# Optimization experiments

Measured on AMD Instinct MI355X. Metric: run time of the kernel, lower is better.

Reference implementation:

```python
import jax, jax.numpy as jnp
import numpy as np
from jax import lax

SEQ = 32768
I = 128   # input_size
H = 512   # hidden_layer_size


def lstm_scan(xs, W_ih, W_hh, b_ih, b_hh):
    """Single-layer LSTM over time (PyTorch gate order i,f,g,o), batch=1.
    xs: [T, in], W_ih: [4h, in], W_hh: [4h, h], biases: [4h]. Returns [T, h]."""
    h_dim = W_hh.shape[1]
    x_gates = xs @ W_ih.T + (b_ih + b_hh)  # precompute input contribution [T, 4h]

    def step(carry, xg):
        h, c = carry
        gates = xg + h @ W_hh.T
        i, f, g, o = jnp.split(gates, 4)
        i = jax.nn.sigmoid(i)
        f = jax.nn.sigmoid(f)
        g = jnp.tanh(g)
        o = jax.nn.sigmoid(o)
        c = f * c + i * g
        h = o * jnp.tanh(c)
        return (h, c), h

    init = (jnp.zeros((h_dim,), xs.dtype), jnp.zeros((h_dim,), xs.dtype))
    _, hs = lax.scan(step, init, x_gates)
    return hs


def setup_inputs() -> dict:
    key = jax.random.key(0)
    ks = jax.random.split(key, 9)
    u = lambda k, shape, fan: jax.random.uniform(k, shape, jnp.float32, -1.0, 1.0) / np.sqrt(fan)
    return {
        "input_seq": jax.random.normal(ks[0], (SEQ, I), jnp.float32),
        # layer 1: input I -> hidden H
        "W_ih1": u(ks[1], (4 * H, I), H),
        "W_hh1": u(ks[2], (4 * H, H), H),
        "b_ih1": u(ks[3], (4 * H,), H),
        "b_hh1": u(ks[4], (4 * H,), H),
        # layer 2: hidden H -> input I
        "W_ih2": u(ks[5], (4 * I, H), I),
        "W_hh2": u(ks[6], (4 * I, I), I),
        "b_ih2": u(ks[7], (4 * I,), I),
        "b_hh2": u(ks[8], (4 * I,), I),
    }


def reference(input_seq, W_ih1, W_hh1, b_ih1, b_hh1, W_ih2, W_hh2, b_ih2, b_hh2):
    h1 = lstm_scan(input_seq, W_ih1, W_hh1, b_ih1, b_hh1)   # [T, H]
    h2 = lstm_scan(h1, W_ih2, W_hh2, b_ih2, b_hh2)          # [T, I]
    return h2.reshape(-1)                                    # predictions.view(-1)
```

## Files before the change

### kernel.cpp

```cpp
#include <hip/hip_runtime.h>
#include <math.h>


#define T_STEPS 32768
#define L1WG    16
#define NWG     24
#define BLK     512
#define GRID    192
#define RD      8

#define ABT_OFF  9
#define TAG_OFF  32
#define H1F_OFF  1024
#define H1S_OFF  (H1F_OFF + RD * 512 * 2)
#define H2F_OFF  (H1S_OFF + RD * 512 * 2)
#define H2S_OFF  (H2F_OFF + RD * 128 * 2)
#define WS_WORDS (H2S_OFF + RD * 128 * 2)

typedef unsigned int uint4v __attribute__((ext_vector_type(4)));

__device__ __forceinline__ float sigm(float x) { return 1.0f / (1.0f + __expf(-x)); }
__device__ __forceinline__ float tanh_fast(float x) { return 1.0f - 2.0f / (__expf(2.0f * x) + 1.0f); }

__device__ __forceinline__ unsigned ld_u32_sc1(const unsigned* p) {
    unsigned r;
    asm volatile("global_load_dword %0, %1, off sc1\n\ts_waitcnt vmcnt(0)"
                 : "=v"(r) : "v"(p) : "memory");
    return r;
}
__device__ __forceinline__ void st_u32_sc1(unsigned* p, unsigned v) {
    asm volatile("global_store_dword %0, %1, off sc1" :: "v"(p), "v"(v) : "memory");
}
__device__ __forceinline__ void st_u64_sc0(unsigned long long* p, unsigned long long v) {
    asm volatile("global_store_dwordx2 %0, %1, off sc0" :: "v"(p), "v"(v) : "memory");
}
__device__ __forceinline__ void st_u64_sc1(unsigned long long* p, unsigned long long v) {
    asm volatile("global_store_dwordx2 %0, %1, off sc1" :: "v"(p), "v"(v) : "memory");
}
__device__ __forceinline__ void ld2x16_sc0(const unsigned long long* p, uint4v& A, uint4v& B) {
    asm volatile("global_load_dwordx4 %0, %2, off sc0\n\t"
                 "global_load_dwordx4 %1, %3, off sc0\n\t"
                 "s_waitcnt vmcnt(0)"
                 : "=&v"(A), "=&v"(B) : "v"(p), "v"(p + 2) : "memory");
}
__device__ __forceinline__ void ld2x16_sc1(const unsigned long long* p, uint4v& A, uint4v& B) {
    asm volatile("global_load_dwordx4 %0, %2, off sc1\n\t"
                 "global_load_dwordx4 %1, %3, off sc1\n\t"
                 "s_waitcnt vmcnt(0)"
                 : "=&v"(A), "=&v"(B) : "v"(p), "v"(p + 2) : "memory");
}
__device__ __forceinline__ void ld1x16_sc0(const unsigned long long* p, uint4v& A) {
    asm volatile("global_load_dwordx4 %0, %1, off sc0\n\ts_waitcnt vmcnt(0)"
                 : "=&v"(A) : "v"(p) : "memory");
}
__device__ __forceinline__ void ld1x16_sc1(const unsigned long long* p, uint4v& A) {
    asm volatile("global_load_dwordx4 %0, %1, off sc1\n\ts_waitcnt vmcnt(0)"
                 : "=&v"(A) : "v"(p) : "memory");
}

__global__ void lstm_init(unsigned int* ws)
{
    int i = blockIdx.x * blockDim.x + threadIdx.x;
    if (i < WS_WORDS) ws[i] = 0u;
}

__global__ __launch_bounds__(BLK) void lstm_persist(
    const float* __restrict__ x,
    const float* __restrict__ Wih1,
    const float* __restrict__ Whh1,
    const float* __restrict__ bih1,
    const float* __restrict__ bhh1,
    const float* __restrict__ Wih2,
    const float* __restrict__ Whh2,
    const float* __restrict__ bih2,
    const float* __restrict__ bhh2,
    float* __restrict__ out,
    unsigned int* ws)
{
    const int bid = blockIdx.x;
    if (bid & 7) return;
    const int role = bid >> 3;
    if (role >= NWG) return;

    const int tid  = threadIdx.x;
    const int wave = tid >> 6;
    const int lane = tid & 63;

    __shared__ __align__(16) float h1buf[2][16 * 36];
    __shared__ __align__(16) float h2buf[2][8 * 20];
    __shared__ unsigned s_ab[1];

    unsigned* abf  = ws + ABT_OFF;
    unsigned* tags = ws + TAG_OFF;
    unsigned long long* h1f = (unsigned long long*)(ws + H1F_OFF);
    unsigned long long* h1s = (unsigned long long*)(ws + H1S_OFF);
    unsigned long long* h2f = (unsigned long long*)(ws + H2F_OFF);
    unsigned long long* h2s = (unsigned long long*)(ws + H2S_OFF);

    if (tid == 0) s_ab[0] = 0u;

    const bool isL1 = role < L1WG;

    if (isL1) {
        const int rt = tid >> 4;
        const int ct = tid & 15;
        const int hb = role * 32;

        float wA[4][32], wB[4][8], bia[4];
#pragma unroll
        for (int q = 0; q < 4; ++q) {
            const int grow = q * 512 + hb + rt;
            const float4* pa = (const float4*)(Whh1 + (size_t)grow * 512 + ct * 32);
#pragma unroll
            for (int c = 0; c < 8; ++c) {
                float4 f = pa[c];
                wA[q][c * 4 + 0] = f.x; wA[q][c * 4 + 1] = f.y;
                wA[q][c * 4 + 2] = f.z; wA[q][c * 4 + 3] = f.w;
            }
            const float4* pb = (const float4*)(Wih1 + (size_t)grow * 128 + ct * 8);
            float4 b0 = pb[0], b1 = pb[1];
            wB[q][0] = b0.x; wB[q][1] = b0.y; wB[q][2] = b0.z; wB[q][3] = b0.w;
            wB[q][4] = b1.x; wB[q][5] = b1.y; wB[q][6] = b1.z; wB[q][7] = b1.w;
            bia[q] = bih1[grow] + bhh1[grow];
        }

        float cst = 0.0f;
        float4 vx0 = *(const float4*)(x + ct * 8);
        float4 vx1 = *(const float4*)(x + ct * 8 + 4);
        __syncthreads();

        for (int n = 0; n < T_STEPS; ++n) {
            if (wave == 3 && n >= 7 && lane < NWG) {
                const int thr = n - 6;
                unsigned sp = 0;
                for (;;) {
                    int ok = ((int)ld_u32_sc1(&tags[lane]) >= thr);
                    if (__all(ok)) break;
                    if ((++sp & 255u) == 0u) {
                        if (ld_u32_sc1(abf) != 0u) { s_ab[0] = 1u; break; }
                        if (sp >= (1u << 21)) { st_u32_sc1(abf, 1u); s_ab[0] = 1u; break; }
                    }
                }
            }
            if (wave < 2) {
                const size_t off = (size_t)((n - 1) & (RD - 1)) * 512 + wave * 256 + lane * 4;
                const unsigned long long* pf = h1f + off;
                const unsigned long long* ps = h1s + off;
                const unsigned e = (unsigned)n;
                uint4v A, B;
                unsigned sp = 0;
                for (;;) {
                    ld2x16_sc0(pf, A, B);
                    int ok = (A.y == e) & (A.w == e) & (B.y == e) & (B.w == e);
                    if (__all(ok)) break;
                    if ((++sp & 7u) == 0u) {
                        uint4v C, D;
                        ld2x16_sc1(ps, C, D);
                        if (A.y != e) { A.x = C.x; A.y = C.y; }
                        if (A.w != e) { A.z = C.z; A.w = C.w; }
                        if (B.y != e) { B.x = D.x; B.y = D.y; }
                        if (B.w != e) { B.z = D.z; B.w = D.w; }
                        ok = (A.y == e) & (A.w == e) & (B.y == e) & (B.w == e);
                        if (__all(ok)) break;
                        if ((sp & 2047u) == 0u) {
                            if (ld_u32_sc1(abf) != 0u) { s_ab[0] = 1u; break; }
                            if (sp >= (1u << 22)) { st_u32_sc1(abf, 1u); s_ab[0] = 1u; break; }
                        }
                    }
                }
                const int g = wave * 256 + lane * 4;
                float4 vals = make_float4(__uint_as_float(A.x), __uint_as_float(A.z),
                                          __uint_as_float(B.x), __uint_as_float(B.z));
                *(float4*)&h1buf[n & 1][(g >> 5) * 36 + (g & 31)] = vals;
            }

            __syncthreads();
            if (s_ab[0]) break;
            if (tid == 0) st_u32_sc1(&tags[role], (unsigned)(n + 1));

            float acc0 = 0.f, acc1 = 0.f, acc2 = 0.f, acc3 = 0.f;
            const float* hv = &h1buf[n & 1][ct * 36];
#pragma unroll
            for (int c = 0; c < 8; ++c) {
                float4 h4 = *(const float4*)(hv + c * 4);
                acc0 = fmaf(wA[0][c*4+0], h4.x, acc0); acc0 = fmaf(wA[0][c*4+1], h4.y, acc0);
                acc0 = fmaf(wA[0][c*4+2], h4.z, acc0); acc0 = fmaf(wA[0][c*4+3], h4.w, acc0);
                acc1 = fmaf(wA[1][c*4+0], h4.x, acc1); acc1 = fmaf(wA[1][c*4+1], h4.y, acc1);
                acc1 = fmaf(wA[1][c*4+2], h4.z, acc1); acc1 = fmaf(wA[1][c*4+3], h4.w, acc1);
                acc2 = fmaf(wA[2][c*4+0], h4.x, acc2); acc2 = fmaf(wA[2][c*4+1], h4.y, acc2);
                acc2 = fmaf(wA[2][c*4+2], h4.z, acc2); acc2 = fmaf(wA[2][c*4+3], h4.w, acc2);
                acc3 = fmaf(wA[3][c*4+0], h4.x, acc3); acc3 = fmaf(wA[3][c*4+1], h4.y, acc3);
                acc3 = fmaf(wA[3][c*4+2], h4.z, acc3); acc3 = fmaf(wA[3][c*4+3], h4.w, acc3);
            }
            {
                float sx[8] = { vx0.x, vx0.y, vx0.z, vx0.w, vx1.x, vx1.y, vx1.z, vx1.w };
#pragma unroll
                for (int j = 0; j < 8; ++j) {
                    acc0 = fmaf(wB[0][j], sx[j], acc0);
                    acc1 = fmaf(wB[1][j], sx[j], acc1);
                    acc2 = fmaf(wB[2][j], sx[j], acc2);
                    acc3 = fmaf(wB[3][j], sx[j], acc3);
                }
            }
            {
                const int tn = (n + 1 < T_STEPS) ? (n + 1) : (T_STEPS - 1);
                vx0 = *(const float4*)(x + (size_t)tn * 128 + ct * 8);
                vx1 = *(const float4*)(x + (size_t)tn * 128 + ct * 8 + 4);
            }
#pragma unroll
            for (int m = 8; m >= 1; m >>= 1) {
                acc0 += __shfl_xor(acc0, m, 64);
                acc1 += __shfl_xor(acc1, m, 64);
                acc2 += __shfl_xor(acc2, m, 64);
                acc3 += __shfl_xor(acc3, m, 64);
            }
            const float ii = sigm(acc0 + bia[0]);
            const float ff = sigm(acc1 + bia[1]);
            const float g2 = tanh_fast(acc2 + bia[2]);
            const float oo = sigm(acc3 + bia[3]);
            cst = ff * cst + ii * g2;
            const float h = oo * tanh_fast(cst);

            if (ct == 0) {
                const unsigned long long pair =
                    ((unsigned long long)(unsigned)(n + 1) << 32) |
                    (unsigned long long)__float_as_uint(h);
                const size_t off = (size_t)(n & (RD - 1)) * 512 + hb + rt;
                st_u64_sc0(&h1f[off], pair);
                st_u64_sc1(&h1s[off], pair);
            }
        }
    } else {
        const int rt  = tid >> 5;
        const int ct  = tid & 31;
        const int hb2 = (role - L1WG) * 16;

        float wA[4][16], wB[4][4], bia[4];
#pragma unroll
        for (int q = 0; q < 4; ++q) {
            const int grow = q * 128 + hb2 + rt;
            const float4* pa = (const float4*)(Wih2 + (size_t)grow * 512 + ct * 16);
#pragma unroll
            for (int c = 0; c < 4; ++c) {
                float4 f = pa[c];
                wA[q][c * 4 + 0] = f.x; wA[q][c * 4 + 1] = f.y;
                wA[q][c * 4 + 2] = f.z; wA[q][c * 4 + 3] = f.w;
            }
            float4 b0 = *(const float4*)(Whh2 + (size_t)grow * 128 + ct * 4);
            wB[q][0] = b0.x; wB[q][1] = b0.y; wB[q][2] = b0.z; wB[q][3] = b0.w;
            bia[q] = bih2[grow] + bhh2[grow];
        }

        float cst = 0.0f;
        __syncthreads();

        for (int n = 1; n <= T_STEPS; ++n) {
            const int tau = n - 1;
            if (wave == 3 && n >= 7 && lane < NWG) {
                const int thr = n - 6;
                unsigned sp = 0;
                for (;;) {
                    int ok = ((int)ld_u32_sc1(&tags[lane]) >= thr);
                    if (__all(ok)) break;
                    if ((++sp & 255u) == 0u) {
                        if (ld_u32_sc1(abf) != 0u) { s_ab[0] = 1u; break; }
                        if (sp >= (1u << 21)) { st_u32_sc1(abf, 1u); s_ab[0] = 1u; break; }
                    }
                }
            }
            if (wave < 2) {
                const size_t off = (size_t)(tau & (RD - 1)) * 512 + wave * 256 + lane * 4;
                const unsigned long long* pf = h1f + off;
                const unsigned long long* ps = h1s + off;
                const unsigned e = (unsigned)n;
                uint4v A, B;
                unsigned sp = 0;
                for (;;) {
                    ld2x16_sc0(pf, A, B);
                    int ok = (A.y == e) & (A.w == e) & (B.y == e) & (B.w == e);
                    if (__all(ok)) break;
                    if ((++sp & 7u) == 0u) {
                        uint4v C, D;
                        ld2x16_sc1(ps, C, D);
                        if (A.y != e) { A.x = C.x; A.y = C.y; }
                        if (A.w != e) { A.z = C.z; A.w = C.w; }
                        if (B.y != e) { B.x = D.x; B.y = D.y; }
                        if (B.w != e) { B.z = D.z; B.w = D.w; }
                        ok = (A.y == e) & (A.w == e) & (B.y == e) & (B.w == e);
                        if (__all(ok)) break;
                        if ((sp & 2047u) == 0u) {
                            if (ld_u32_sc1(abf) != 0u) { s_ab[0] = 1u; break; }
                            if (sp >= (1u << 22)) { st_u32_sc1(abf, 1u); s_ab[0] = 1u; break; }
                        }
                    }
                }
                const int g = wave * 256 + lane * 4;
                float4 vals = make_float4(__uint_as_float(A.x), __uint_as_float(A.z),
                                          __uint_as_float(B.x), __uint_as_float(B.z));
                *(float4*)&h1buf[n & 1][(g >> 5) * 36 + (g & 31)] = vals;
            }
            if (wave == 2) {
                const size_t off = (size_t)((tau - 1) & (RD - 1)) * 128 + lane * 2;
                const unsigned long long* pf = h2f + off;
                const unsigned long long* ps = h2s + off;
                const unsigned e = (unsigned)tau;
                uint4v A;
                unsigned sp = 0;
                for (;;) {
                    ld1x16_sc0(pf, A);
                    int ok = (A.y == e) & (A.w == e);
                    if (__all(ok)) break;
                    if ((++sp & 7u) == 0u) {
                        uint4v C;
                        ld1x16_sc1(ps, C);
                        if (A.y != e) { A.x = C.x; A.y = C.y; }
                        if (A.w != e) { A.z = C.z; A.w = C.w; }
                        ok = (A.y == e) & (A.w == e);
                        if (__all(ok)) break;
                        if ((sp & 2047u) == 0u) {
                            if (ld_u32_sc1(abf) != 0u) { s_ab[0] = 1u; break; }
                            if (sp >= (1u << 22)) { st_u32_sc1(abf, 1u); s_ab[0] = 1u; break; }
                        }
                    }
                }
                const int pi = lane * 2;
                float2 v2 = make_float2(__uint_as_float(A.x), __uint_as_float(A.z));
                *(float2*)&h2buf[n & 1][(pi >> 4) * 20 + (pi & 15)] = v2;
            }

            __syncthreads();
            if (s_ab[0]) break;
            if (tid == 0) st_u32_sc1(&tags[role], (unsigned)(n + 1));

            float acc0 = 0.f, acc1 = 0.f, acc2 = 0.f, acc3 = 0.f;
            const float* hv = &h1buf[n & 1][(ct >> 1) * 36 + (ct & 1) * 16];
#pragma unroll
            for (int c = 0; c < 4; ++c) {
                float4 h4 = *(const float4*)(hv + c * 4);
                acc0 = fmaf(wA[0][c*4+0], h4.x, acc0); acc0 = fmaf(wA[0][c*4+1], h4.y, acc0);
                acc0 = fmaf(wA[0][c*4+2], h4.z, acc0); acc0 = fmaf(wA[0][c*4+3], h4.w, acc0);
                acc1 = fmaf(wA[1][c*4+0], h4.x, acc1); acc1 = fmaf(wA[1][c*4+1], h4.y, acc1);
                acc1 = fmaf(wA[1][c*4+2], h4.z, acc1); acc1 = fmaf(wA[1][c*4+3], h4.w, acc1);
                acc2 = fmaf(wA[2][c*4+0], h4.x, acc2); acc2 = fmaf(wA[2][c*4+1], h4.y, acc2);
                acc2 = fmaf(wA[2][c*4+2], h4.z, acc2); acc2 = fmaf(wA[2][c*4+3], h4.w, acc2);
                acc3 = fmaf(wA[3][c*4+0], h4.x, acc3); acc3 = fmaf(wA[3][c*4+1], h4.y, acc3);
                acc3 = fmaf(wA[3][c*4+2], h4.z, acc3); acc3 = fmaf(wA[3][c*4+3], h4.w, acc3);
            }
            {
                float4 s4 = *(const float4*)&h2buf[n & 1][(ct >> 2) * 20 + (ct & 3) * 4];
                float sv[4] = { s4.x, s4.y, s4.z, s4.w };
#pragma unroll
                for (int j = 0; j < 4; ++j) {
                    acc0 = fmaf(wB[0][j], sv[j], acc0);
                    acc1 = fmaf(wB[1][j], sv[j], acc1);
                    acc2 = fmaf(wB[2][j], sv[j], acc2);
                    acc3 = fmaf(wB[3][j], sv[j], acc3);
                }
            }
#pragma unroll
            for (int m = 16; m >= 1; m >>= 1) {
                acc0 += __shfl_xor(acc0, m, 64);
                acc1 += __shfl_xor(acc1, m, 64);
                acc2 += __shfl_xor(acc2, m, 64);
                acc3 += __shfl_xor(acc3, m, 64);
            }
            const float ii = sigm(acc0 + bia[0]);
            const float ff = sigm(acc1 + bia[1]);
            const float g2 = tanh_fast(acc2 + bia[2]);
            const float oo = sigm(acc3 + bia[3]);
            cst = ff * cst + ii * g2;
            const float h = oo * tanh_fast(cst);

            if (ct == 0) {
                const unsigned long long pair =
                    ((unsigned long long)(unsigned)n << 32) |
                    (unsigned long long)__float_as_uint(h);
                const size_t off = (size_t)(tau & (RD - 1)) * 128 + hb2 + rt;
                st_u64_sc0(&h2f[off], pair);
                st_u64_sc1(&h2s[off], pair);
                out[(size_t)tau * 128 + hb2 + rt] = h;
            }
        }
    }
}

extern "C" void kernel_launch(void* const* d_in, const int* in_sizes, int n_in,
                              void* d_out, int out_size, void* d_ws, size_t ws_size,
                              hipStream_t stream)
{
    const float* x    = (const float*)d_in[0];
    const float* Wih1 = (const float*)d_in[1];
    const float* Whh1 = (const float*)d_in[2];
    const float* bih1 = (const float*)d_in[3];
    const float* bhh1 = (const float*)d_in[4];
    const float* Wih2 = (const float*)d_in[5];
    const float* Whh2 = (const float*)d_in[6];
    const float* bih2 = (const float*)d_in[7];
    const float* bhh2 = (const float*)d_in[8];
    unsigned int* ws  = (unsigned int*)d_ws;

    hipLaunchKernelGGL(lstm_init, dim3(96), dim3(256), 0, stream, ws);
    hipLaunchKernelGGL(lstm_persist, dim3(GRID), dim3(BLK), 0, stream,
                       x, Wih1, Whh1, bih1, bhh1, Wih2, Whh2, bih2, bhh2,
                       (float*)d_out, ws);
}
```

Before: 87.85 ms.

## Co-locate all persistent workgroups on one XCD and batch ring-slack checks

Roles are no longer assigned from a fixed block-id stride. Each workgroup reads its XCC id from a hardware register and takes a ticket from a per-XCD atomic counter, and the first XCD to fill all 24 roles wins. This keeps every cross-workgroup flag and h-exchange inside one XCD's L2 rather than crossing dies, which should cut inter-step handoff latency. The grid grows to 256 blocks so one XCD is likely to get 24 of them. The ring-buffer slack wait now runs every 4 steps with threshold n-3 instead of every step with n-6, so it polls less often. In exchange, the assignment adds a startup spin, and if no XCD ever fills the roles, no workgroup takes a role.

```diff
diff --git a/kernel.cpp b/kernel.cpp
--- a/kernel.cpp
+++ b/kernel.cpp
@@ -6,9 +6,11 @@
 #define L1WG    16
 #define NWG     24
 #define BLK     512
-#define GRID    192
+#define GRID    256
 #define RD      8
 
+#define CNT_OFF  0
+#define CHO_OFF  8
 #define ABT_OFF  9
 #define TAG_OFF  32
 #define H1F_OFF  1024
@@ -77,19 +79,17 @@
     float* __restrict__ out,
     unsigned int* ws)
 {
-    const int bid = blockIdx.x;
-    if (bid & 7) return;
-    const int role = bid >> 3;
-    if (role >= NWG) return;
-
     const int tid  = threadIdx.x;
     const int wave = tid >> 6;
     const int lane = tid & 63;
 
     __shared__ __align__(16) float h1buf[2][16 * 36];
     __shared__ __align__(16) float h2buf[2][8 * 20];
+    __shared__ unsigned s_role[1];
     __shared__ unsigned s_ab[1];
 
+    unsigned* cnt  = ws + CNT_OFF;
+    unsigned* cho  = ws + CHO_OFF;
     unsigned* abf  = ws + ABT_OFF;
     unsigned* tags = ws + TAG_OFF;
     unsigned long long* h1f = (unsigned long long*)(ws + H1F_OFF);
@@ -97,7 +97,34 @@
     unsigned long long* h2f = (unsigned long long*)(ws + H2F_OFF);
     unsigned long long* h2s = (unsigned long long*)(ws + H2S_OFF);
 
-    if (tid == 0) s_ab[0] = 0u;
+    if (tid == 0) {
+        s_ab[0] = 0u;
+        unsigned xcc;
+        asm volatile("s_getreg_b32 %0, hwreg(20, 0, 32)" : "=s"(xcc));
+        xcc &= 7u;
+        unsigned role = 0xFFFFu;
+        unsigned tkt = __hip_atomic_fetch_add(&cnt[xcc], 1u,
+                           __ATOMIC_RELAXED, __HIP_MEMORY_SCOPE_AGENT);
+        if (tkt < NWG) {
+            if (tkt == NWG - 1) {
+                unsigned exp = 0u;
+                __hip_atomic_compare_exchange_strong(cho, &exp, xcc + 1u,
+                    __ATOMIC_RELAXED, __ATOMIC_RELAXED, __HIP_MEMORY_SCOPE_AGENT);
+            }
+            unsigned c, sp = 0;
+            for (;;) {
+                c = __hip_atomic_load(cho, __ATOMIC_RELAXED, __HIP_MEMORY_SCOPE_AGENT);
+                if (c != 0u) break;
+                __builtin_amdgcn_s_sleep(2);
+                if (++sp > (1u << 22)) { c = 0xFFu; break; }
+            }
+            if (c == xcc + 1u) role = tkt;
+        }
+        s_role[0] = role;
+    }
+    __syncthreads();
+    const int role = (int)s_role[0];
+    if (role >= NWG) return;
 
     const bool isL1 = role < L1WG;
 
@@ -130,8 +157,8 @@
         __syncthreads();
 
         for (int n = 0; n < T_STEPS; ++n) {
-            if (wave == 3 && n >= 7 && lane < NWG) {
-                const int thr = n - 6;
+            if (wave == 3 && n >= 8 && (n & 3) == 0 && lane < NWG) {
+                const int thr = n - 3;
                 unsigned sp = 0;
                 for (;;) {
                     int ok = ((int)ld_u32_sc1(&tags[lane]) >= thr);
@@ -256,8 +283,8 @@
 
         for (int n = 1; n <= T_STEPS; ++n) {
             const int tau = n - 1;
-            if (wave == 3 && n >= 7 && lane < NWG) {
-                const int thr = n - 6;
+            if (wave == 3 && n >= 8 && (n & 3) == 0 && lane < NWG) {
+                const int thr = n - 3;
                 unsigned sp = 0;
                 for (;;) {
                     int ok = ((int)ld_u32_sc1(&tags[lane]) >= thr);
```

Result: no change. 86.83 ms (-1.2%).

## Use single sc1 ring buffers, per-lane spin with early LDS write, relaxed tag throttling

Applied to the files above, without the earlier changes.

Drops the duplicated fast/slow (sc0/sc1) ring buffers and publishes each hidden value once with an sc1 store. Consumers now poll only the sc1 copy, and each lane writes its value to LDS as soon as its tag matches. The change also checks the run-ahead tags only every fourth step with a tighter lag. It launches exactly 24 blocks instead of 192 with most returning early, and pins weight registers with empty asm. The aim is to cut polling traffic and per-step synchronisation latency. The cost is possible extra cache round-trips from sc1-only loads, and blocks may no longer be spread across distinct XCDs/CUs.

```diff
diff --git a/kernel.cpp b/kernel.cpp
--- a/kernel.cpp
+++ b/kernel.cpp
@@ -6,18 +6,17 @@
 #define L1WG    16
 #define NWG     24
 #define BLK     512
-#define GRID    192
 #define RD      8
 
 #define ABT_OFF  9
 #define TAG_OFF  32
-#define H1F_OFF  1024
-#define H1S_OFF  (H1F_OFF + RD * 512 * 2)
-#define H2F_OFF  (H1S_OFF + RD * 512 * 2)
-#define H2S_OFF  (H2F_OFF + RD * 128 * 2)
-#define WS_WORDS (H2S_OFF + RD * 128 * 2)
+#define H1_OFF   1024
+#define H2_OFF   (H1_OFF + RD * 512 * 2)
+#define WS_WORDS (H2_OFF + RD * 128 * 2)
 
 typedef unsigned int uint4v __attribute__((ext_vector_type(4)));
+
+#define PIN(v) asm volatile("" : "+v"(v))
 
 __device__ __forceinline__ float sigm(float x) { return 1.0f / (1.0f + __expf(-x)); }
 __device__ __forceinline__ float tanh_fast(float x) { return 1.0f - 2.0f / (__expf(2.0f * x) + 1.0f); }
@@ -31,17 +30,8 @@
 __device__ __forceinline__ void st_u32_sc1(unsigned* p, unsigned v) {
     asm volatile("global_store_dword %0, %1, off sc1" :: "v"(p), "v"(v) : "memory");
 }
-__device__ __forceinline__ void st_u64_sc0(unsigned long long* p, unsigned long long v) {
-    asm volatile("global_store_dwordx2 %0, %1, off sc0" :: "v"(p), "v"(v) : "memory");
-}
 __device__ __forceinline__ void st_u64_sc1(unsigned long long* p, unsigned long long v) {
     asm volatile("global_store_dwordx2 %0, %1, off sc1" :: "v"(p), "v"(v) : "memory");
-}
-__device__ __forceinline__ void ld2x16_sc0(const unsigned long long* p, uint4v& A, uint4v& B) {
-    asm volatile("global_load_dwordx4 %0, %2, off sc0\n\t"
-                 "global_load_dwordx4 %1, %3, off sc0\n\t"
-                 "s_waitcnt vmcnt(0)"
-                 : "=&v"(A), "=&v"(B) : "v"(p), "v"(p + 2) : "memory");
 }
 __device__ __forceinline__ void ld2x16_sc1(const unsigned long long* p, uint4v& A, uint4v& B) {
     asm volatile("global_load_dwordx4 %0, %2, off sc1\n\t"
@@ -49,10 +39,6 @@
                  "s_waitcnt vmcnt(0)"
                  : "=&v"(A), "=&v"(B) : "v"(p), "v"(p + 2) : "memory");
 }
-__device__ __forceinline__ void ld1x16_sc0(const unsigned long long* p, uint4v& A) {
-    asm volatile("global_load_dwordx4 %0, %1, off sc0\n\ts_waitcnt vmcnt(0)"
-                 : "=&v"(A) : "v"(p) : "memory");
-}
 __device__ __forceinline__ void ld1x16_sc1(const unsigned long long* p, uint4v& A) {
     asm volatile("global_load_dwordx4 %0, %1, off sc1\n\ts_waitcnt vmcnt(0)"
                  : "=&v"(A) : "v"(p) : "memory");
@@ -64,7 +50,7 @@
     if (i < WS_WORDS) ws[i] = 0u;
 }
 
-__global__ __launch_bounds__(BLK) void lstm_persist(
+__global__ __launch_bounds__(BLK, 2) void lstm_persist(
     const float* __restrict__ x,
     const float* __restrict__ Wih1,
     const float* __restrict__ Whh1,
@@ -77,11 +63,7 @@
     float* __restrict__ out,
     unsigned int* ws)
 {
-    const int bid = blockIdx.x;
-    if (bid & 7) return;
-    const int role = bid >> 3;
-    if (role >= NWG) return;
-
+    const int role = blockIdx.x;
     const int tid  = threadIdx.x;
     const int wave = tid >> 6;
     const int lane = tid & 63;
@@ -92,10 +74,8 @@
 
     unsigned* abf  = ws + ABT_OFF;
     unsigned* tags = ws + TAG_OFF;
-    unsigned long long* h1f = (unsigned long long*)(ws + H1F_OFF);
-    unsigned long long* h1s = (unsigned long long*)(ws + H1S_OFF);
-    unsigned long long* h2f = (unsigned long long*)(ws + H2F_OFF);
-    unsigned long long* h2s = (unsigned long long*)(ws + H2S_OFF);
+    unsigned long long* h1r = (unsigned long long*)(ws + H1_OFF);
+    unsigned long long* h2r = (unsigned long long*)(ws + H2_OFF);
 
     if (tid == 0) s_ab[0] = 0u;
 
@@ -123,6 +103,14 @@
             wB[q][4] = b1.x; wB[q][5] = b1.y; wB[q][6] = b1.z; wB[q][7] = b1.w;
             bia[q] = bih1[grow] + bhh1[grow];
         }
+#pragma unroll
+        for (int q = 0; q < 4; ++q) {
+#pragma unroll
+            for (int j = 0; j < 32; ++j) PIN(wA[q][j]);
+#pragma unroll
+            for (int j = 0; j < 8; ++j)  PIN(wB[q][j]);
+            PIN(bia[q]);
+        }
 
         float cst = 0.0f;
         float4 vx0 = *(const float4*)(x + ct * 8);
@@ -130,8 +118,8 @@
         __syncthreads();
 
         for (int n = 0; n < T_STEPS; ++n) {
-            if (wave == 3 && n >= 7 && lane < NWG) {
-                const int thr = n - 6;
+            if (wave == 3 && n >= 8 && (n & 3) == 0 && lane < NWG) {
+                const int thr = n - 3;
                 unsigned sp = 0;
                 for (;;) {
                     int ok = ((int)ld_u32_sc1(&tags[lane]) >= thr);
@@ -144,34 +132,29 @@
             }
             if (wave < 2) {
                 const size_t off = (size_t)((n - 1) & (RD - 1)) * 512 + wave * 256 + lane * 4;
-                const unsigned long long* pf = h1f + off;
-                const unsigned long long* ps = h1s + off;
+                const unsigned long long* p = h1r + off;
                 const unsigned e = (unsigned)n;
-                uint4v A, B;
-                unsigned sp = 0;
-                for (;;) {
-                    ld2x16_sc0(pf, A, B);
-                    int ok = (A.y == e) & (A.w == e) & (B.y == e) & (B.w == e);
-                    if (__all(ok)) break;
-                    if ((++sp & 7u) == 0u) {
-                        uint4v C, D;
-                        ld2x16_sc1(ps, C, D);
-                        if (A.y != e) { A.x = C.x; A.y = C.y; }
-                        if (A.w != e) { A.z = C.z; A.w = C.w; }
-                        if (B.y != e) { B.x = D.x; B.y = D.y; }
-                        if (B.w != e) { B.z = D.z; B.w = D.w; }
-                        ok = (A.y == e) & (A.w == e) & (B.y == e) & (B.w == e);
-                        if (__all(ok)) break;
-                        if ((sp & 2047u) == 0u) {
-                            if (ld_u32_sc1(abf) != 0u) { s_ab[0] = 1u; break; }
-                            if (sp >= (1u << 22)) { st_u32_sc1(abf, 1u); s_ab[0] = 1u; break; }
+                const int g = wave * 256 + lane * 4;
+                bool done = false;
+                unsigned sp = 0;
+                for (;;) {
+                    if (!done) {
+                        uint4v A, B;
+                        ld2x16_sc1(p, A, B);
+                        if ((A.y == e) & (A.w == e) & (B.y == e) & (B.w == e)) {
+                            float4 vals = make_float4(
+                                __uint_as_float(A.x), __uint_as_float(A.z),
+                                __uint_as_float(B.x), __uint_as_float(B.z));
+                            *(float4*)&h1buf[n & 1][(g >> 5) * 36 + (g & 31)] = vals;
+                            done = true;
                         }
                     }
-                }
-                const int g = wave * 256 + lane * 4;
-                float4 vals = make_float4(__uint_as_float(A.x), __uint_as_float(A.z),
-                                          __uint_as_float(B.x), __uint_as_float(B.z));
-                *(float4*)&h1buf[n & 1][(g >> 5) * 36 + (g & 31)] = vals;
+                    if (__all(done)) break;
+                    if ((++sp & 255u) == 0u) {
+                        if (ld_u32_sc1(abf) != 0u) { s_ab[0] = 1u; break; }
+                        if (sp >= (1u << 21)) { st_u32_sc1(abf, 1u); s_ab[0] = 1u; break; }
+                    }
+                }
             }
 
             __syncthreads();
@@ -225,9 +208,7 @@
                 const unsigned long long pair =
                     ((unsigned long long)(unsigned)(n + 1) << 32) |
                     (unsigned long long)__float_as_uint(h);
-                const size_t off = (size_t)(n & (RD - 1)) * 512 + hb + rt;
-                st_u64_sc0(&h1f[off], pair);
-                st_u64_sc1(&h1s[off], pair);
+                st_u64_sc1(&h1r[(size_t)(n & (RD - 1)) * 512 + hb + rt], pair);
             }
         }
     } else {
@@ -250,14 +231,22 @@
             wB[q][0] = b0.x; wB[q][1] = b0.y; wB[q][2] = b0.z; wB[q][3] = b0.w;
             bia[q] = bih2[grow] + bhh2[grow];
         }
+#pragma unroll
+        for (int q = 0; q < 4; ++q) {
+#pragma unroll
+            for (int j = 0; j < 16; ++j) PIN(wA[q][j]);
+#pragma unroll
+            for (int j = 0; j < 4; ++j)  PIN(wB[q][j]);
+            PIN(bia[q]);
+        }
 
         float cst = 0.0f;
         __syncthreads();
 
         for (int n = 1; n <= T_STEPS; ++n) {
             const int tau = n - 1;
-            if (wave == 3 && n >= 7 && lane < NWG) {
-                const int thr = n - 6;
+            if (wave == 3 && n >= 8 && (n & 3) == 0 && lane < NWG) {
+                const int thr = n - 3;
                 unsigned sp = 0;
                 for (;;) {
                     int ok = ((int)ld_u32_sc1(&tags[lane]) >= thr);
@@ -270,62 +259,54 @@
             }
             if (wave < 2) {
                 const size_t off = (size_t)(tau & (RD - 1)) * 512 + wave * 256 + lane * 4;
-                const unsigned long long* pf = h1f + off;
-                const unsigned long long* ps = h1s + off;
+                const unsigned long long* p = h1r + off;
                 const unsigned e = (unsigned)n;
-                uint4v A, B;
-                unsigned sp = 0;
-                for (;;) {
-                    ld2x16_sc0(pf, A, B);
-                    int ok = (A.y == e) & (A.w == e) & (B.y == e) & (B.w == e);
-                    if (__all(ok)) break;
-                    if ((++sp & 7u) == 0u) {
-                        uint4v C, D;
-                        ld2x16_sc1(ps, C, D);
-                        if (A.y != e) { A.x = C.x; A.y = C.y; }
-                        if (A.w != e) { A.z = C.z; A.w = C.w; }
-                        if (B.y != e) { B.x = D.x; B.y = D.y; }
-                        if (B.w != e) { B.z = D.z; B.w = D.w; }
-                        ok = (A.y == e) & (A.w == e) & (B.y == e) & (B.w == e);
-                        if (__all(ok)) break;
-                        if ((sp & 2047u) == 0u) {
-                            if (ld_u32_sc1(abf) != 0u) { s_ab[0] = 1u; break; }
-                            if (sp >= (1u << 22)) { st_u32_sc1(abf, 1u); s_ab[0] = 1u; break; }
+                const int g = wave * 256 + lane * 4;
+                bool done = false;
+                unsigned sp = 0;
+                for (;;) {
+                    if (!done) {
+                        uint4v A, B;
+                        ld2x16_sc1(p, A, B);
+                        if ((A.y == e) & (A.w == e) & (B.y == e) & (B.w == e)) {
+                            float4 vals = make_float4(
+                                __uint_as_float(A.x), __uint_as_float(A.z),
+                                __uint_as_float(B.x), __uint_as_float(B.z));
+                            *(float4*)&h1buf[n & 1][(g >> 5) * 36 + (g & 31)] = vals;
+                            done = true;
                         }
                     }
-                }
-                const int g = wave * 256 + lane * 4;
-                float4 vals = make_float4(__uint_as_float(A.x), __uint_as_float(A.z),
-                                          __uint_as_float(B.x), __uint_as_float(B.z));
-                *(float4*)&h1buf[n & 1][(g >> 5) * 36 + (g & 31)] = vals;
+                    if (__all(done)) break;
+                    if ((++sp & 255u) == 0u) {
+                        if (ld_u32_sc1(abf) != 0u) { s_ab[0] = 1u; break; }
+                        if (sp >= (1u << 21)) { st_u32_sc1(abf, 1u); s_ab[0] = 1u; break; }
+                    }
+                }
             }
             if (wave == 2) {
                 const size_t off = (size_t)((tau - 1) & (RD - 1)) * 128 + lane * 2;
-                const unsigned long long* pf = h2f + off;
-                const unsigned long long* ps = h2s + off;
+                const unsigned long long* p = h2r + off;
                 const unsigned e = (unsigned)tau;
-                uint4v A;
-                unsigned sp = 0;
-                for (;;) {
-                    ld1x16_sc0(pf, A);
-                    int ok = (A.y == e) & (A.w == e);
-                    if (__all(ok)) break;
-                    if ((++sp & 7u) == 0u) {
-                        uint4v C;
-                        ld1x16_sc1(ps, C);
-                        if (A.y != e) { A.x = C.x; A.y = C.y; }
-                        if (A.w != e) { A.z = C.z; A.w = C.w; }
-                        ok = (A.y == e) & (A.w == e);
-                        if (__all(ok)) break;
-                        if ((sp & 2047u) == 0u) {
-                            if (ld_u32_sc1(abf) != 0u) { s_ab[0] = 1u; break; }
-                            if (sp >= (1u << 22)) { st_u32_sc1(abf, 1u); s_ab[0] = 1u; break; }
+                const int pi = lane * 2;
+                bool done = false;
+                unsigned sp = 0;
+                for (;;) {
+                    if (!done) {
+                        uint4v A;
+                        ld1x16_sc1(p, A);
+                        if ((A.y == e) & (A.w == e)) {
+                            float2 v2 = make_float2(__uint_as_float(A.x),
+                                                    __uint_as_float(A.z));
+                            *(float2*)&h2buf[n & 1][(pi >> 4) * 20 + (pi & 15)] = v2;
+                            done = true;
                         }
                     }
-                }
-                const int pi = lane * 2;
-                float2 v2 = make_float2(__uint_as_float(A.x), __uint_as_float(A.z));
-                *(float2*)&h2buf[n & 1][(pi >> 4) * 20 + (pi & 15)] = v2;
+                    if (__all(done)) break;
+                    if ((++sp & 255u) == 0u) {
+                        if (ld_u32_sc1(abf) != 0u) { s_ab[0] = 1u; break; }
+                        if (sp >= (1u << 21)) { st_u32_sc1(abf, 1u); s_ab[0] = 1u; break; }
+                    }
+                }
             }
 
             __syncthreads();
@@ -375,9 +356,7 @@
                 const unsigned long long pair =
                     ((unsigned long long)(unsigned)n << 32) |
                     (unsigned long long)__float_as_uint(h);
-                const size_t off = (size_t)(tau & (RD - 1)) * 128 + hb2 + rt;
-                st_u64_sc0(&h2f[off], pair);
-                st_u64_sc1(&h2s[off], pair);
+                st_u64_sc1(&h2r[(size_t)(tau & (RD - 1)) * 128 + hb2 + rt], pair);
                 out[(size_t)tau * 128 + hb2 + rt] = h;
             }
         }
@@ -399,8 +378,8 @@
     const float* bhh2 = (const float*)d_in[8];
     unsigned int* ws  = (unsigned int*)d_ws;
 
-    hipLaunchKernelGGL(lstm_init, dim3(96), dim3(256), 0, stream, ws);
-    hipLaunchKernelGGL(lstm_persist, dim3(GRID), dim3(BLK), 0, stream,
+    hipLaunchKernelGGL(lstm_init, dim3(44), dim3(256), 0, stream, ws);
+    hipLaunchKernelGGL(lstm_persist, dim3(NWG), dim3(BLK), 0, stream,
                        x, Wih1, Whh1, bih1, bhh1, Wih2, Whh2, bih2, bhh2,
                        (float*)d_out, ws);
 }
```

Result: slower. 90.95 ms (+3.5%).

## Split layer-1 across 32 workgroups and launch exactly NWG blocks

Applied to the files above, without the earlier changes.

Layer 1's hidden dimension is now spread over 32 workgroups of 16 rows each instead of 16 of 32, so each thread holds half as many weights and runs a shorter dot product with a 32-lane reduction. The grid launches exactly 40 blocks instead of 192 with most exiting early, and launch bounds allow 2 blocks per CU, which removes the earlier one-block-per-8 spacing trick and may let blocks share CUs. The cross-workgroup tag throttle check now runs every 4th step with a tighter lag window, cutting global polling traffic. More participants raise the cost of each per-step handshake and may add contention.

```diff
diff --git a/kernel.cpp b/kernel.cpp
--- a/kernel.cpp
+++ b/kernel.cpp
@@ -3,10 +3,9 @@
 
 
 #define T_STEPS 32768
-#define L1WG    16
-#define NWG     24
+#define L1WG    32
+#define NWG     40
 #define BLK     512
-#define GRID    192
 #define RD      8
 
 #define ABT_OFF  9
@@ -64,7 +63,7 @@
     if (i < WS_WORDS) ws[i] = 0u;
 }
 
-__global__ __launch_bounds__(BLK) void lstm_persist(
+__global__ __launch_bounds__(BLK, 2) void lstm_persist(
     const float* __restrict__ x,
     const float* __restrict__ Wih1,
     const float* __restrict__ Whh1,
@@ -77,16 +76,12 @@
     float* __restrict__ out,
     unsigned int* ws)
 {
-    const int bid = blockIdx.x;
-    if (bid & 7) return;
-    const int role = bid >> 3;
-    if (role >= NWG) return;
-
+    const int role = blockIdx.x;
     const int tid  = threadIdx.x;
     const int wave = tid >> 6;
     const int lane = tid & 63;
 
-    __shared__ __align__(16) float h1buf[2][16 * 36];
+    __shared__ __align__(16) float h1buf[2][32 * 20];
     __shared__ __align__(16) float h2buf[2][8 * 20];
     __shared__ unsigned s_ab[1];
 
@@ -100,38 +95,35 @@
     if (tid == 0) s_ab[0] = 0u;
 
     const bool isL1 = role < L1WG;
+    const int rt = tid >> 5;
+    const int ct = tid & 31;
 
     if (isL1) {
-        const int rt = tid >> 4;
-        const int ct = tid & 15;
-        const int hb = role * 32;
-
-        float wA[4][32], wB[4][8], bia[4];
+        const int hb = role * 16;
+
+        float wA[4][16], wB[4][4], bia[4];
 #pragma unroll
         for (int q = 0; q < 4; ++q) {
             const int grow = q * 512 + hb + rt;
-            const float4* pa = (const float4*)(Whh1 + (size_t)grow * 512 + ct * 32);
-#pragma unroll
-            for (int c = 0; c < 8; ++c) {
+            const float4* pa = (const float4*)(Whh1 + (size_t)grow * 512 + ct * 16);
+#pragma unroll
+            for (int c = 0; c < 4; ++c) {
                 float4 f = pa[c];
                 wA[q][c * 4 + 0] = f.x; wA[q][c * 4 + 1] = f.y;
                 wA[q][c * 4 + 2] = f.z; wA[q][c * 4 + 3] = f.w;
             }
-            const float4* pb = (const float4*)(Wih1 + (size_t)grow * 128 + ct * 8);
-            float4 b0 = pb[0], b1 = pb[1];
-            wB[q][0] = b0.x; wB[q][1] = b0.y; wB[q][2] = b0.z; wB[q][3] = b0.w;
-            wB[q][4] = b1.x; wB[q][5] = b1.y; wB[q][6] = b1.z; wB[q][7] = b1.w;
+            float4 fb = *(const float4*)(Wih1 + (size_t)grow * 128 + ct * 4);
+            wB[q][0] = fb.x; wB[q][1] = fb.y; wB[q][2] = fb.z; wB[q][3] = fb.w;
             bia[q] = bih1[grow] + bhh1[grow];
         }
 
         float cst = 0.0f;
-        float4 vx0 = *(const float4*)(x + ct * 8);
-        float4 vx1 = *(const float4*)(x + ct * 8 + 4);
+        float4 vx = *(const float4*)(x + ct * 4);
         __syncthreads();
 
         for (int n = 0; n < T_STEPS; ++n) {
-            if (wave == 3 && n >= 7 && lane < NWG) {
-                const int thr = n - 6;
+            if (wave == 3 && n >= 8 && (n & 3) == 0 && lane < NWG) {
+                const int thr = n - 3;
                 unsigned sp = 0;
                 for (;;) {
                     int ok = ((int)ld_u32_sc1(&tags[lane]) >= thr);
@@ -171,7 +163,7 @@
                 const int g = wave * 256 + lane * 4;
                 float4 vals = make_float4(__uint_as_float(A.x), __uint_as_float(A.z),
                                           __uint_as_float(B.x), __uint_as_float(B.z));
-                *(float4*)&h1buf[n & 1][(g >> 5) * 36 + (g & 31)] = vals;
+                *(float4*)&h1buf[n & 1][(g >> 4) * 20 + (g & 15)] = vals;
             }
 
             __syncthreads();
@@ -179,9 +171,9 @@
             if (tid == 0) st_u32_sc1(&tags[role], (unsigned)(n + 1));
 
             float acc0 = 0.f, acc1 = 0.f, acc2 = 0.f, acc3 = 0.f;
-            const float* hv = &h1buf[n & 1][ct * 36];
-#pragma unroll
-            for (int c = 0; c < 8; ++c) {
+            const float* hv = &h1buf[n & 1][ct * 20];
+#pragma unroll
+            for (int c = 0; c < 4; ++c) {
                 float4 h4 = *(const float4*)(hv + c * 4);
                 acc0 = fmaf(wA[0][c*4+0], h4.x, acc0); acc0 = fmaf(wA[0][c*4+1], h4.y, acc0);
                 acc0 = fmaf(wA[0][c*4+2], h4.z, acc0); acc0 = fmaf(wA[0][c*4+3], h4.w, acc0);
@@ -193,9 +185,9 @@
                 acc3 = fmaf(wA[3][c*4+2], h4.z, acc3); acc3 = fmaf(wA[3][c*4+3], h4.w, acc3);
             }
             {
-                float sx[8] = { vx0.x, vx0.y, vx0.z, vx0.w, vx1.x, vx1.y, vx1.z, vx1.w };
-#pragma unroll
-                for (int j = 0; j < 8; ++j) {
+                const float sx[4] = { vx.x, vx.y, vx.z, vx.w };
+#pragma unroll
+                for (int j = 0; j < 4; ++j) {
                     acc0 = fmaf(wB[0][j], sx[j], acc0);
                     acc1 = fmaf(wB[1][j], sx[j], acc1);
                     acc2 = fmaf(wB[2][j], sx[j], acc2);
@@ -204,11 +196,10 @@
             }
             {
                 const int tn = (n + 1 < T_STEPS) ? (n + 1) : (T_STEPS - 1);
-                vx0 = *(const float4*)(x + (size_t)tn * 128 + ct * 8);
-                vx1 = *(const float4*)(x + (size_t)tn * 128 + ct * 8 + 4);
-            }
-#pragma unroll
-            for (int m = 8; m >= 1; m >>= 1) {
+                vx = *(const float4*)(x + (size_t)tn * 128 + ct * 4);
+            }
+#pragma unroll
+            for (int m = 16; m >= 1; m >>= 1) {
                 acc0 += __shfl_xor(acc0, m, 64);
                 acc1 += __shfl_xor(acc1, m, 64);
                 acc2 += __shfl_xor(acc2, m, 64);
@@ -231,8 +222,6 @@
             }
         }
     } else {
-        const int rt  = tid >> 5;
-        const int ct  = tid & 31;
         const int hb2 = (role - L1WG) * 16;
 
         float wA[4][16], wB[4][4], bia[4];
@@ -256,8 +245,8 @@
 
         for (int n = 1; n <= T_STEPS; ++n) {
             const int tau = n - 1;
-            if (wave == 3 && n >= 7 && lane < NWG) {
-                const int thr = n - 6;
+            if (wave == 3 && n >= 8 && (n & 3) == 0 && lane < NWG) {
+                const int thr = n - 3;
                 unsigned sp = 0;
                 for (;;) {
                     int ok = ((int)ld_u32_sc1(&tags[lane]) >= thr);
@@ -297,7 +286,7 @@
                 const int g = wave * 256 + lane * 4;
                 float4 vals = make_float4(__uint_as_float(A.x), __uint_as_float(A.z),
                                           __uint_as_float(B.x), __uint_as_float(B.z));
-                *(float4*)&h1buf[n & 1][(g >> 5) * 36 + (g & 31)] = vals;
+                *(float4*)&h1buf[n & 1][(g >> 4) * 20 + (g & 15)] = vals;
             }
             if (wave == 2) {
                 const size_t off = (size_t)((tau - 1) & (RD - 1)) * 128 + lane * 2;
@@ -333,7 +322,7 @@
             if (tid == 0) st_u32_sc1(&tags[role], (unsigned)(n + 1));
 
             float acc0 = 0.f, acc1 = 0.f, acc2 = 0.f, acc3 = 0.f;
-            const float* hv = &h1buf[n & 1][(ct >> 1) * 36 + (ct & 1) * 16];
+            const float* hv = &h1buf[n & 1][ct * 20];
 #pragma unroll
             for (int c = 0; c < 4; ++c) {
                 float4 h4 = *(const float4*)(hv + c * 4);
@@ -348,7 +337,7 @@
             }
             {
                 float4 s4 = *(const float4*)&h2buf[n & 1][(ct >> 2) * 20 + (ct & 3) * 4];
-                float sv[4] = { s4.x, s4.y, s4.z, s4.w };
+                const float sv[4] = { s4.x, s4.y, s4.z, s4.w };
 #pragma unroll
                 for (int j = 0; j < 4; ++j) {
                     acc0 = fmaf(wB[0][j], sv[j], acc0);
@@ -400,7 +389,7 @@
     unsigned int* ws  = (unsigned int*)d_ws;
 
     hipLaunchKernelGGL(lstm_init, dim3(96), dim3(256), 0, stream, ws);
-    hipLaunchKernelGGL(lstm_persist, dim3(GRID), dim3(BLK), 0, stream,
+    hipLaunchKernelGGL(lstm_persist, dim3(NWG), dim3(BLK), 0, stream,
                        x, Wih1, Whh1, bih1, bhh1, Wih2, Whh2, bih2, bhh2,
                        (float*)d_out, ws);
 }
```

Result: slower. 93.01 ms (+5.9%).
